# Performance work log

Measured on AMD Instinct MI355X. Metric: run time of the kernel, lower is better.

The kernel has to match this reference:

```python
import jax, jax.numpy as jnp
from jax import lax
import numpy as np

EPS = 1e-5  # BatchNorm2d default eps

def _cbs(x, w, g, b, m, v, pad):
    # Conv2d(bias=False) + BatchNorm2d (eval mode, running stats) + SiLU
    y = lax.conv_general_dilated(x, w, (1, 1), [(pad, pad), (pad, pad)],
                                 dimension_numbers=('NCHW', 'OIHW', 'NCHW'))
    y = (y - m[None, :, None, None]) * (g / jnp.sqrt(v + EPS))[None, :, None, None] + b[None, :, None, None]
    return y * jax.nn.sigmoid(y)

def setup_inputs():
    key = jax.random.key(0)
    B, C1, C2, H, W = 2, 128, 128, 20, 20
    ks = iter(jax.random.split(key, 16))
    def wconv(o, i, s):
        return jax.random.normal(next(ks), (o, i, s, s), jnp.float32) / np.float32(np.sqrt(i * s * s))
    def bn(cdim):
        k1, k2 = jax.random.split(next(ks))
        g = jax.random.uniform(k1, (cdim,), jnp.float32, 0.5, 1.5)
        b = jax.random.normal(k2, (cdim,), jnp.float32) * 0.1
        return g, b, jnp.zeros((cdim,), jnp.float32), jnp.ones((cdim,), jnp.float32)
    inp = {'x': jax.random.normal(next(ks), (B, C1, H, W), jnp.float32)}
    inp['w1'] = wconv(C2, C1, 1); inp['g1'], inp['b1'], inp['m1'], inp['v1'] = bn(C2)
    inp['w2'] = wconv(C2, C1, 1); inp['g2'], inp['b2'], inp['m2'], inp['v2'] = bn(C2)
    inp['wr1'] = wconv(C2, 2 * C2, 1); inp['gr1'], inp['br1'], inp['mr1'], inp['vr1'] = bn(C2)
    inp['wr2'] = wconv(C2, C2, 3); inp['gr2'], inp['br2'], inp['mr2'], inp['vr2'] = bn(C2)
    inp['wr3'] = wconv(1, C2, 1); inp['gr3'], inp['br3'], inp['mr3'], inp['vr3'] = bn(1)
    return inp

def reference(x, w1, g1, b1, m1, v1, w2, g2, b2, m2, v2,
              wr1, gr1, br1, mr1, vr1, wr2, gr2, br2, mr2, vr2,
              wr3, gr3, br3, mr3, vr3):
    B, C, H, W = x.shape
    HW = H * W
    # feat: [B, HW, C2]
    feat = _cbs(x, w1, g1, b1, m1, v1, 0).reshape(B, -1, HW).transpose(0, 2, 1)
    C2 = feat.shape[-1]
    # pairwise concat: rel[b,i,j] = [feat[b,i], feat[b,j]]  -> [B, HW, HW, 2*C2]
    fi = jnp.broadcast_to(feat[:, :, None, :], (B, HW, HW, C2))
    fj = jnp.broadcast_to(feat[:, None, :, :], (B, HW, HW, C2))
    rel = jnp.concatenate([fi, fj], axis=-1)
    # faithful permute(0,3,1,2) + contiguous view to [B*HW, 2*C2, H, W]
    rel = rel.transpose(0, 3, 1, 2).reshape(B * HW, 2 * C2, H, W)
    r = _cbs(rel, wr1, gr1, br1, mr1, vr1, 0)
    r = _cbs(r, wr2, gr2, br2, mr2, vr2, 1)
    r = _cbs(r, wr3, gr3, br3, mr3, vr3, 0)  # [B*HW, 1, H, W]
    scores = r.reshape(B, HW, HW)
    # bmm aggregation then back to [B, C2, H, W]
    att = jnp.einsum('bij,bjc->bic', scores, feat).transpose(0, 2, 1).reshape(B, C2, H, W)
    return _cbs(att, w2, g2, b2, m2, v2, 0) + x
```

## Files before the change

kernel.cpp:

```cpp
#include <hip/hip_runtime.h>

#define EPS 1e-5f

typedef __bf16 bf16x8 __attribute__((ext_vector_type(8)));
typedef float  f32x4  __attribute__((ext_vector_type(4)));

__device__ __forceinline__ unsigned short f2bf(float f) {
  unsigned int u = __float_as_uint(f);
  unsigned int r = (u + 0x7fffu + ((u >> 16) & 1u)) >> 16;
  return (unsigned short)r;
}
__device__ __forceinline__ float silu(float y) { return y / (1.f + __expf(-y)); }

__global__ void prep_kernel(const float* __restrict__ x, const float* __restrict__ w1,
                            const float* __restrict__ g1, const float* __restrict__ b1,
                            const float* __restrict__ m1, const float* __restrict__ v1,
                            const float* __restrict__ wr2, const float* __restrict__ wr1,
                            float* __restrict__ feat, float* __restrict__ attz,
                            unsigned short* __restrict__ Apack, float* __restrict__ Pfx,
                            float* __restrict__ Wt) {
  int blk = blockIdx.x;
  int tid = threadIdx.x;
  if (blk < 400) {
    int hp = tid >> 7, c = tid & 127;
    int pp = blk * 2 + hp;
    int b = pp / 400, p = pp % 400;
    __shared__ float xv[2][128];
    xv[hp][c] = x[(b * 128 + c) * 400 + p];
    __syncthreads();
    const float4* w4 = (const float4*)(w1 + c * 128);
    const float4* v4 = (const float4*)xv[hp];
    float s0 = 0.f, s1 = 0.f, s2 = 0.f, s3 = 0.f;
#pragma unroll
    for (int i = 0; i < 32; ++i) {
      float4 wv = w4[i], xx = v4[i];
      s0 += wv.x * xx.x; s1 += wv.y * xx.y; s2 += wv.z * xx.z; s3 += wv.w * xx.w;
    }
    float s = (s0 + s1) + (s2 + s3);
    float sc = g1[c] * rsqrtf(v1[c] + EPS);
    float y = s * sc + (b1[c] - m1[c] * sc);
    int o = (b * 400 + p) * 128 + c;
    feat[o] = silu(y);
    if (p >= 200) attz[o] = 0.f;
  } else if (blk < 472) {
    int f = (blk - 400) * 4 + (tid >> 6);
    int lane = tid & 63;
    int tap = f >> 5, ks = (f >> 3) & 3, m8 = f & 7;
    int o  = m8 * 16 + (lane & 15);
    int cb = ks * 32 + (lane >> 4) * 8;
    unsigned short* dst = Apack + ((size_t)f * 64 + lane) * 8;
#pragma unroll
    for (int j = 0; j < 8; ++j)
      dst[j] = f2bf(wr2[(o * 128 + (cb + j)) * 9 + tap]);
  } else if (blk < 504) {
    int o = (blk - 472) * 4 + (tid >> 6);
    int lane = tid & 63;
    float4 wv = ((const float4*)(wr1 + o * 256))[lane];
    float p0 = wv.x, p1 = p0 + wv.y, p2 = p1 + wv.z, p3 = p2 + wv.w;
    float v = p3;
#pragma unroll
    for (int d = 1; d < 64; d <<= 1) {
      float t = __shfl_up(v, d);
      if (lane >= d) v += t;
    }
    float off = v - p3;
    float* Po = Pfx + o * 257;
    if (lane == 0) Po[0] = 0.f;
    Po[lane * 4 + 1] = off + p0;
    Po[lane * 4 + 2] = off + p1;
    Po[lane * 4 + 3] = off + p2;
    Po[lane * 4 + 4] = off + p3;
  } else {
    int base = (blk - 504) * 1024;
#pragma unroll
    for (int k = 0; k < 4; ++k) {
      int idx = base + k * 256 + tid;
      int tap = idx >> 14;
      int r = idx & 16383;
      int i = r >> 7, o = r & 127;
      Wt[idx] = wr2[(o * 128 + i) * 9 + tap];
    }
  }
}

__global__ __launch_bounds__(512, 4) void rel_kernel(
    const float* __restrict__ feat, const float* __restrict__ wr1, const float* __restrict__ Pfx,
    const float* __restrict__ gr1, const float* __restrict__ br1,
    const float* __restrict__ mr1, const float* __restrict__ vr1,
    const unsigned short* __restrict__ Apack, const float* __restrict__ Wt,
    const float* __restrict__ gr2, const float* __restrict__ br2,
    const float* __restrict__ mr2, const float* __restrict__ vr2,
    const float* __restrict__ wr3,
    const float* __restrict__ gr3, const float* __restrict__ br3,
    const float* __restrict__ mr3, const float* __restrict__ vr3,
    float* __restrict__ att) {

  __shared__ __align__(16) unsigned short r1f[16 * 221 * 8];
  __shared__ float f0s[220], f1s[220], scoreS[208];
  __shared__ float wB0s[128], wB1s[128];
  __shared__ float sc1[128], sh1[128], sc2[128], sh2[128], w3c[128];
  __shared__ float attT[128];
  __shared__ float fA[256], r1c[128], AvS[128];
  __shared__ float vS[9 * 128];
  __shared__ float spS[9];
  __shared__ float spP[400];

  int tid = threadIdx.x, lane = tid & 63, wid = tid >> 6;
  int blk = blockIdx.x;

  if (tid < 128) {
    float s1 = gr1[tid] * rsqrtf(vr1[tid] + EPS); sc1[tid] = s1; sh1[tid] = br1[tid] - mr1[tid] * s1;
    float s2 = gr2[tid] * rsqrtf(vr2[tid] + EPS); sc2[tid] = s2; sh2[tid] = br2[tid] - mr2[tid] * s2;
    w3c[tid] = wr3[tid];
    attT[tid] = 0.f; AvS[tid] = 0.f;
  }
  float s3 = gr3[0] * rsqrtf(vr3[0] + EPS);
  float sh3 = br3[0] - mr3[0] * s3;

  if (blk < 800) {
    int idx = blk >> 1, half = blk & 1;
    int b = idx / 200, q = 200 + idx % 200;
    int c0 = (q * 256) / 400, c1 = c0 + 1;
    if (tid < 128) {
      const float* Po = Pfx + tid * 257;
      int e0 = min(256, 400 * c0 + 400 - 256 * q);
      wB0s[tid] = Po[e0];
      float wv = 0.f;
      if (c1 < 256) {
        int s1i = min(256, max(0, 400 * c1 - 256 * q));
        wv = Po[256] - Po[s1i];
      }
      wB1s[tid] = wv;
    }
    if (tid < 220) {
      int p = tid + 180 * half;
      f0s[tid] = feat[(b * 400 + p) * 128 + (c0 - 128)];
      f1s[tid] = (c1 < 256) ? feat[(b * 400 + p) * 128 + (c1 - 128)] : 0.f;
    }
    if (tid < 208) scoreS[tid] = 0.f;
    __syncthreads();

    for (int i = tid; i < 3520; i += 512) {
      int plane = i / 220, p = i - plane * 220;
      int cb = (plane >> 2) * 32 + (plane & 3) * 8;
      float fa0 = f0s[p], fa1 = f1s[p];
      unsigned int pk[4];
#pragma unroll
      for (int jp = 0; jp < 4; ++jp) {
        int c = cb + jp * 2;
        float y0 = wB0s[c] * fa0 + wB1s[c] * fa1;     y0 = y0 * sc1[c] + sh1[c];
        float y1 = wB0s[c + 1] * fa0 + wB1s[c + 1] * fa1; y1 = y1 * sc1[c + 1] + sh1[c + 1];
        pk[jp] = (unsigned int)f2bf(silu(y0)) | ((unsigned int)f2bf(silu(y1)) << 16);
      }
      *(uint4*)&r1f[(plane * 221 + p) * 8] = make_uint4(pk[0], pk[1], pk[2], pk[3]);
    }
    if (tid < 16) *(uint4*)&r1f[(tid * 221 + 220) * 8] = make_uint4(0, 0, 0, 0);

    int wm = wid & 1, wn = wid >> 1;
    int ntcnt = (wn == 0) ? 4 : 3;
    int n16 = lane & 15, quad = lane >> 4;
    int hA[4], wA[4], poA[4]; bool pov[4];
#pragma unroll
    for (int t = 0; t < 4; ++t) {
      int po = (wn + 4 * t) * 16 + n16;
      poA[t] = po; pov[t] = po < 200;
      int pg = half * 200 + po;
      hA[t] = pg / 20; wA[t] = pg - 20 * hA[t];
    }
    f32x4 acc[4][4];
#pragma unroll
    for (int mt = 0; mt < 4; ++mt)
#pragma unroll
      for (int t = 0; t < 4; ++t) acc[mt][t] = f32x4{0.f, 0.f, 0.f, 0.f};

    __syncthreads();

    const char* wbase = (const char*)Apack + (size_t)((wm * 4) * 64 + lane) * 16;
    for (int tap = 0; tap < 9; ++tap) {
      int dy = tap / 3 - 1, dx = tap % 3 - 1;
      int pp[4];
#pragma unroll
      for (int t = 0; t < 4; ++t) {
        int hh = hA[t] + dy, ww = wA[t] + dx;
        bool valid = pov[t] & (hh >= 0) & (hh < 20) & (ww >= 0) & (ww < 20);
        pp[t] = valid ? (hh - 9 * half) * 20 + ww : 220;
      }
#pragma unroll
      for (int ks = 0; ks < 4; ++ks) {
        const char* wp = wbase + (size_t)(tap * 4 + ks) * 8192;
        bf16x8 af0 = *(const bf16x8*)(wp);
        bf16x8 af1 = *(const bf16x8*)(wp + 1024);
        bf16x8 af2 = *(const bf16x8*)(wp + 2048);
        bf16x8 af3 = *(const bf16x8*)(wp + 3072);
        int pbase = (ks * 4 + quad) * 221;
#pragma unroll
        for (int t = 0; t < 4; ++t) {
          if (t < ntcnt) {
            bf16x8 bfr = *(const bf16x8*)&r1f[(pbase + pp[t]) * 8];
            acc[0][t] = __builtin_amdgcn_mfma_f32_16x16x32_bf16(af0, bfr, acc[0][t], 0, 0, 0);
            acc[1][t] = __builtin_amdgcn_mfma_f32_16x16x32_bf16(af1, bfr, acc[1][t], 0, 0, 0);
            acc[2][t] = __builtin_amdgcn_mfma_f32_16x16x32_bf16(af2, bfr, acc[2][t], 0, 0, 0);
            acc[3][t] = __builtin_amdgcn_mfma_f32_16x16x32_bf16(af3, bfr, acc[3][t], 0, 0, 0);
          }
        }
      }
    }

#pragma unroll
    for (int t = 0; t < 4; ++t) {
      if (t < ntcnt) {
        float ps = 0.f;
#pragma unroll
        for (int mt = 0; mt < 4; ++mt) {
#pragma unroll
          for (int r = 0; r < 4; ++r) {
            int o = wm * 64 + mt * 16 + quad * 4 + r;
            float y = acc[mt][t][r] * sc2[o] + sh2[o];
            ps += silu(y) * w3c[o];
          }
        }
        ps += __shfl_xor(ps, 16);
        ps += __shfl_xor(ps, 32);
        if (quad == 0 && pov[t]) atomicAdd(&scoreS[poA[t]], ps);
      }
    }
    __syncthreads();

    if (tid < 200) scoreS[tid] = silu(scoreS[tid] * s3 + sh3);
    __syncthreads();

    {
      int c = tid & 127, part = tid >> 7;
      float s = 0.f;
      int j0 = part * 50;
      for (int j = j0; j < j0 + 50; ++j)
        s += scoreS[j] * feat[(b * 400 + half * 200 + j) * 128 + c];
      atomicAdd(&attT[c], s);
    }
    __syncthreads();
    if (tid < 128)
      atomicAdd(&att[((size_t)(b * 400 + q)) * 128 + tid], attT[tid]);
  } else {
    int cidx = blk - 800;
    int b = cidx / 200, q = cidx % 200;
    if (tid < 256) {
      int u = q * 256 + tid; int c = u / 400, i2 = u - c * 400;
      fA[tid] = feat[(b * 400 + i2) * 128 + c];
    }
    for (int k = tid; k < 1152; k += 512) vS[k] = 0.f;
    __syncthreads();
    {
      int o = tid & 127, part = tid >> 7;
      const float* wr = wr1 + o * 256 + part * 64;
      const float* fv = fA + part * 64;
      float a = 0.f;
#pragma unroll 8
      for (int k = 0; k < 64; ++k) a += wr[k] * fv[k];
      atomicAdd(&AvS[o], a);
    }
    __syncthreads();
    if (tid < 128) r1c[tid] = silu(AvS[tid] * sc1[tid] + sh1[tid]);
    __syncthreads();
    {
      int o = tid & 127, part = tid >> 7;
      const float* rc = r1c + part * 32;
      for (int tap = 0; tap < 9; ++tap) {
        const float* wt = Wt + tap * 16384 + part * 32 * 128 + o;
        float s = 0.f;
#pragma unroll 8
        for (int i2 = 0; i2 < 32; ++i2) s += wt[i2 * 128] * rc[i2];
        atomicAdd(&vS[tap * 128 + o], s);
      }
    }
    __syncthreads();
    for (int pat = wid; pat < 9; pat += 8) {
      int ry = pat / 3, rx = pat % 3;
      float ps = 0.f;
      for (int oo = lane; oo < 128; oo += 64) {
        float y = 0.f;
#pragma unroll
        for (int dy = -1; dy <= 1; ++dy) {
          if ((ry == 0 && dy < 0) || (ry == 2 && dy > 0)) continue;
#pragma unroll
          for (int dx = -1; dx <= 1; ++dx) {
            if ((rx == 0 && dx < 0) || (rx == 2 && dx > 0)) continue;
            y += vS[((dy + 1) * 3 + (dx + 1)) * 128 + oo];
          }
        }
        y = y * sc2[oo] + sh2[oo];
        ps += silu(y) * w3c[oo];
      }
#pragma unroll
      for (int sft = 32; sft >= 1; sft >>= 1) ps += __shfl_xor(ps, sft);
      if (lane == 0) spS[pat] = silu(ps * s3 + sh3);
    }
    __syncthreads();

    for (int p = tid; p < 400; p += 512) {
      int r = p / 20, cm = p - 20 * r;
      int ry = (r == 0) ? 0 : (r == 19) ? 2 : 1;
      int rx = (cm == 0) ? 0 : (cm == 19) ? 2 : 1;
      spP[p] = spS[ry * 3 + rx];
    }
    __syncthreads();
    {
      int c = tid & 127, part = tid >> 7;
      const float* fb = feat + ((size_t)(b * 400) + part * 100) * 128 + c;
      const float* sp = spP + part * 100;
      float s = 0.f;
      for (int j = 0; j < 100; ++j) s += sp[j] * fb[(size_t)j * 128];
      atomicAdd(&attT[c], s);
    }
    __syncthreads();
    if (tid < 128)
      att[((size_t)(b * 400 + q)) * 128 + tid] = attT[tid];
  }
}

__global__ void out_kernel(const float* __restrict__ att, const float* __restrict__ x,
                           const float* __restrict__ w2,
                           const float* __restrict__ g2, const float* __restrict__ b2,
                           const float* __restrict__ m2, const float* __restrict__ v2,
                           float* __restrict__ out) {
  int pp = blockIdx.x;
  int b = pp / 400, p = pp % 400;
  int tid = threadIdx.x;
  __shared__ float av[128];
  if (tid < 128) av[tid] = att[(size_t)(b * 400 + p) * 128 + tid];
  __syncthreads();
  int c = tid >> 1, part = tid & 1;
  const float4* w4 = (const float4*)(w2 + c * 128 + part * 64);
  const float4* v4 = (const float4*)(av + part * 64);
  float s0 = 0.f, s1 = 0.f, s2 = 0.f, s3 = 0.f;
#pragma unroll
  for (int i = 0; i < 16; ++i) {
    float4 wv = w4[i], xx = v4[i];
    s0 += wv.x * xx.x; s1 += wv.y * xx.y; s2 += wv.z * xx.z; s3 += wv.w * xx.w;
  }
  float s = (s0 + s1) + (s2 + s3);
  s += __shfl_xor(s, 1);
  if (part == 0) {
    float sc = g2[c] * rsqrtf(v2[c] + EPS);
    float y = s * sc + (b2[c] - m2[c] * sc);
    int xi = (b * 128 + c) * 400 + p;
    out[xi] = silu(y) + x[xi];
  }
}

extern "C" void kernel_launch(void* const* d_in, const int* in_sizes, int n_in,
                              void* d_out, int out_size, void* d_ws, size_t ws_size,
                              hipStream_t stream) {
  const float* x   = (const float*)d_in[0];
  const float* w1  = (const float*)d_in[1];
  const float* g1  = (const float*)d_in[2];
  const float* b1  = (const float*)d_in[3];
  const float* m1  = (const float*)d_in[4];
  const float* v1  = (const float*)d_in[5];
  const float* w2  = (const float*)d_in[6];
  const float* g2  = (const float*)d_in[7];
  const float* b2  = (const float*)d_in[8];
  const float* m2  = (const float*)d_in[9];
  const float* v2  = (const float*)d_in[10];
  const float* wr1 = (const float*)d_in[11];
  const float* gr1 = (const float*)d_in[12];
  const float* br1 = (const float*)d_in[13];
  const float* mr1 = (const float*)d_in[14];
  const float* vr1 = (const float*)d_in[15];
  const float* wr2 = (const float*)d_in[16];
  const float* gr2 = (const float*)d_in[17];
  const float* br2 = (const float*)d_in[18];
  const float* mr2 = (const float*)d_in[19];
  const float* vr2 = (const float*)d_in[20];
  const float* wr3 = (const float*)d_in[21];
  const float* gr3 = (const float*)d_in[22];
  const float* br3 = (const float*)d_in[23];
  const float* mr3 = (const float*)d_in[24];
  const float* vr3 = (const float*)d_in[25];
  float* out = (float*)d_out;

  char* ws = (char*)d_ws;
  float*          feat  = (float*)ws;
  float*          attb  = (float*)(ws + 409600);
  unsigned short* Apack = (unsigned short*)(ws + 819200);
  float*          Pfx   = (float*)(ws + 1114112);
  float*          Wt    = (float*)(ws + 1245696);

  prep_kernel<<<648, 256, 0, stream>>>(x, w1, g1, b1, m1, v1, wr2, wr1,
                                       feat, attb, Apack, Pfx, Wt);
  rel_kernel<<<1200, 512, 0, stream>>>(feat, wr1, Pfx, gr1, br1, mr1, vr1,
                                       Apack, Wt,
                                       gr2, br2, mr2, vr2, wr3, gr3, br3, mr3, vr3, attb);
  out_kernel<<<800, 256, 0, stream>>>(attb, x, w2, g2, b2, m2, v2, out);
}
```

Baseline: 213.5 us.

## Fuse output conv into rel kernel using last-arriver atomic flags

Removes the separate output kernel by computing the final 1x1 conv, BN, SiLU and residual inside rel_kernel. Rows split across two blocks use a per-row atomic counter so that the second block to finish loads the accumulated attention and writes the output. Rows handled by a single block do it directly. w2 is transposed in prep_kernel for coalesced reads, and SiLU now uses a hardware reciprocal. This saves one launch and a global round trip, but adds fences, atomics and extra register and LDS pressure to the heavy kernel.

```diff
diff --git a/kernel.cpp b/kernel.cpp
--- a/kernel.cpp
+++ b/kernel.cpp
@@ -10,18 +10,23 @@
   unsigned int r = (u + 0x7fffu + ((u >> 16) & 1u)) >> 16;
   return (unsigned short)r;
 }
-__device__ __forceinline__ float silu(float y) { return y / (1.f + __expf(-y)); }
+__device__ __forceinline__ float silu(float y) {
+  return y * __builtin_amdgcn_rcpf(1.f + __expf(-y));
+}
 
 __global__ void prep_kernel(const float* __restrict__ x, const float* __restrict__ w1,
                             const float* __restrict__ g1, const float* __restrict__ b1,
                             const float* __restrict__ m1, const float* __restrict__ v1,
                             const float* __restrict__ wr2, const float* __restrict__ wr1,
+                            const float* __restrict__ w2,
                             float* __restrict__ feat, float* __restrict__ attz,
                             unsigned short* __restrict__ Apack, float* __restrict__ Pfx,
-                            float* __restrict__ Wt) {
+                            float* __restrict__ Wt, float* __restrict__ W2t,
+                            int* __restrict__ flags) {
   int blk = blockIdx.x;
   int tid = threadIdx.x;
   if (blk < 400) {
+    if (tid < 2) flags[blk * 2 + tid] = 0;
     int hp = tid >> 7, c = tid & 127;
     int pp = blk * 2 + hp;
     int b = pp / 400, p = pp % 400;
@@ -70,7 +75,7 @@
     Po[lane * 4 + 2] = off + p1;
     Po[lane * 4 + 3] = off + p2;
     Po[lane * 4 + 4] = off + p3;
-  } else {
+  } else if (blk < 648) {
     int base = (blk - 504) * 1024;
 #pragma unroll
     for (int k = 0; k < 4; ++k) {
@@ -80,6 +85,10 @@
       int i = r >> 7, o = r & 127;
       Wt[idx] = wr2[(o * 128 + i) * 9 + tap];
     }
+  } else {
+    int idx = (blk - 648) * 256 + tid;
+    int i = idx >> 7, o = idx & 127;
+    W2t[idx] = w2[o * 128 + i];
   }
 }
 
@@ -93,17 +102,21 @@
     const float* __restrict__ wr3,
     const float* __restrict__ gr3, const float* __restrict__ br3,
     const float* __restrict__ mr3, const float* __restrict__ vr3,
-    float* __restrict__ att) {
+    const float* __restrict__ W2t, const float* __restrict__ g2,
+    const float* __restrict__ b2, const float* __restrict__ m2,
+    const float* __restrict__ v2, const float* __restrict__ x,
+    float* __restrict__ att, float* __restrict__ out, int* __restrict__ flags) {
 
   __shared__ __align__(16) unsigned short r1f[16 * 221 * 8];
   __shared__ float f0s[220], f1s[220], scoreS[208];
   __shared__ float wB0s[128], wB1s[128];
   __shared__ float sc1[128], sh1[128], sc2[128], sh2[128], w3c[128];
-  __shared__ float attT[128];
+  __shared__ float attT[128], outT[128];
   __shared__ float fA[256], r1c[128], AvS[128];
   __shared__ float vS[9 * 128];
   __shared__ float spS[9];
   __shared__ float spP[400];
+  __shared__ int   secondFlag;
 
   int tid = threadIdx.x, lane = tid & 63, wid = tid >> 6;
   int blk = blockIdx.x;
@@ -112,7 +125,7 @@
     float s1 = gr1[tid] * rsqrtf(vr1[tid] + EPS); sc1[tid] = s1; sh1[tid] = br1[tid] - mr1[tid] * s1;
     float s2 = gr2[tid] * rsqrtf(vr2[tid] + EPS); sc2[tid] = s2; sh2[tid] = br2[tid] - mr2[tid] * s2;
     w3c[tid] = wr3[tid];
-    attT[tid] = 0.f; AvS[tid] = 0.f;
+    attT[tid] = 0.f; outT[tid] = 0.f; AvS[tid] = 0.f;
   }
   float s3 = gr3[0] * rsqrtf(vr3[0] + EPS);
   float sh3 = br3[0] - mr3[0] * s3;
@@ -120,6 +133,7 @@
   if (blk < 800) {
     int idx = blk >> 1, half = blk & 1;
     int b = idx / 200, q = 200 + idx % 200;
+    int row = b * 400 + q;
     int c0 = (q * 256) / 400, c1 = c0 + 1;
     if (tid < 128) {
       const float* Po = Pfx + tid * 257;
@@ -239,7 +253,34 @@
     }
     __syncthreads();
     if (tid < 128)
-      atomicAdd(&att[((size_t)(b * 400 + q)) * 128 + tid], attT[tid]);
+      atomicAdd(&att[(size_t)row * 128 + tid], attT[tid]);
+    __syncthreads();
+    if (tid == 0) {
+      __threadfence();
+      secondFlag = (atomicAdd(&flags[row], 1) == 1);
+    }
+    __syncthreads();
+
+    if (secondFlag) {
+      if (tid < 128)
+        attT[tid] = __hip_atomic_load(&att[(size_t)row * 128 + tid],
+                                      __ATOMIC_RELAXED, __HIP_MEMORY_SCOPE_AGENT);
+      __syncthreads();
+      int c = tid & 127, part = tid >> 7;
+      const float* wt = W2t + part * 32 * 128 + c;
+      const float* af = attT + part * 32;
+      float s = 0.f;
+#pragma unroll 8
+      for (int k = 0; k < 32; ++k) s += wt[k * 128] * af[k];
+      atomicAdd(&outT[c], s);
+      __syncthreads();
+      if (tid < 128) {
+        float sc = g2[tid] * rsqrtf(v2[tid] + EPS);
+        float y = outT[tid] * sc + (b2[tid] - m2[tid] * sc);
+        int xi = (b * 128 + tid) * 400 + q;
+        out[xi] = silu(y) + x[xi];
+      }
+    }
   } else {
     int cidx = blk - 800;
     int b = cidx / 200, q = cidx % 200;
@@ -312,38 +353,23 @@
       atomicAdd(&attT[c], s);
     }
     __syncthreads();
-    if (tid < 128)
-      att[((size_t)(b * 400 + q)) * 128 + tid] = attT[tid];
-  }
-}
-
-__global__ void out_kernel(const float* __restrict__ att, const float* __restrict__ x,
-                           const float* __restrict__ w2,
-                           const float* __restrict__ g2, const float* __restrict__ b2,
-                           const float* __restrict__ m2, const float* __restrict__ v2,
-                           float* __restrict__ out) {
-  int pp = blockIdx.x;
-  int b = pp / 400, p = pp % 400;
-  int tid = threadIdx.x;
-  __shared__ float av[128];
-  if (tid < 128) av[tid] = att[(size_t)(b * 400 + p) * 128 + tid];
-  __syncthreads();
-  int c = tid >> 1, part = tid & 1;
-  const float4* w4 = (const float4*)(w2 + c * 128 + part * 64);
-  const float4* v4 = (const float4*)(av + part * 64);
-  float s0 = 0.f, s1 = 0.f, s2 = 0.f, s3 = 0.f;
-#pragma unroll
-  for (int i = 0; i < 16; ++i) {
-    float4 wv = w4[i], xx = v4[i];
-    s0 += wv.x * xx.x; s1 += wv.y * xx.y; s2 += wv.z * xx.z; s3 += wv.w * xx.w;
-  }
-  float s = (s0 + s1) + (s2 + s3);
-  s += __shfl_xor(s, 1);
-  if (part == 0) {
-    float sc = g2[c] * rsqrtf(v2[c] + EPS);
-    float y = s * sc + (b2[c] - m2[c] * sc);
-    int xi = (b * 128 + c) * 400 + p;
-    out[xi] = silu(y) + x[xi];
+
+    {
+      int c = tid & 127, part = tid >> 7;
+      const float* wt = W2t + part * 32 * 128 + c;
+      const float* af = attT + part * 32;
+      float s = 0.f;
+#pragma unroll 8
+      for (int k = 0; k < 32; ++k) s += wt[k * 128] * af[k];
+      atomicAdd(&outT[c], s);
+    }
+    __syncthreads();
+    if (tid < 128) {
+      float sc = g2[tid] * rsqrtf(v2[tid] + EPS);
+      float y = outT[tid] * sc + (b2[tid] - m2[tid] * sc);
+      int xi = (b * 128 + tid) * 400 + q;
+      out[xi] = silu(y) + x[xi];
+    }
   }
 }
 
@@ -384,11 +410,13 @@
   unsigned short* Apack = (unsigned short*)(ws + 819200);
   float*          Pfx   = (float*)(ws + 1114112);
   float*          Wt    = (float*)(ws + 1245696);
-
-  prep_kernel<<<648, 256, 0, stream>>>(x, w1, g1, b1, m1, v1, wr2, wr1,
-                                       feat, attb, Apack, Pfx, Wt);
+  float*          W2t   = (float*)(ws + 1835520);
+  int*            flags = (int*)(ws + 1901056);
+
+  prep_kernel<<<712, 256, 0, stream>>>(x, w1, g1, b1, m1, v1, wr2, wr1, w2,
+                                       feat, attb, Apack, Pfx, Wt, W2t, flags);
   rel_kernel<<<1200, 512, 0, stream>>>(feat, wr1, Pfx, gr1, br1, mr1, vr1,
                                        Apack, Wt,
-                                       gr2, br2, mr2, vr2, wr3, gr3, br3, mr3, vr3, attb);
-  out_kernel<<<800, 256, 0, stream>>>(attb, x, w2, g2, b2, m2, v2, out);
+                                       gr2, br2, mr2, vr2, wr3, gr3, br3, mr3, vr3,
+                                       W2t, g2, b2, m2, v2, x, attb, out, flags);
 }
```

After: 222.0 us. 4.0% more time.
